# Kernel optimization log

Hardware: AMD Instinct MI355X
Metric: run time of the kernel (lower is better)

## Reference

```python
import jax, jax.numpy as jnp
import numpy as np

B, C, H, W = 4, 3, 512, 960
K2 = 16  # 4x4 adaptive filter, DAIN-style


def setup_inputs() -> dict:
    key = jax.random.key(0)
    k1, k2, k3 = jax.random.split(key, 3)
    teninput = jax.random.normal(k1, (B, C, H, W), dtype=jnp.float32)
    tenflow = jax.random.normal(k2, (B, 2, H, W), dtype=jnp.float32)
    tenfilter = jax.random.uniform(k3, (B, K2, H, W), dtype=jnp.float32)
    return {"teninput": teninput, "tenflow": tenflow, "tenfilter": tenfilter}


def reference(teninput, tenflow, tenfilter):
    # DAIN FilterInterpolation forward:
    # out[b,c,y,x] = valid * sum_{dj,di < K} filter[b, dj*K+di, y, x]
    #               * bilinear(input, y2_T + dj + beta, x2_L + di + alpha)
    # with per-corner clamped gathers; out-of-bounds flow targets give 0.
    b, c, h, w = teninput.shape
    k2 = tenfilter.shape[1]
    K = int(np.sqrt(k2))

    dt = teninput.dtype
    xs = jnp.arange(w, dtype=dt)[None, None, :]
    ys = jnp.arange(h, dtype=dt)[None, :, None]
    fx, fy = tenflow[:, 0], tenflow[:, 1]          # [B,H,W]
    x2 = xs + fx
    y2 = ys + fy
    valid = ((x2 >= 0) & (x2 <= w - 1) & (y2 >= 0) & (y2 <= h - 1)
             & (jnp.abs(fx) < w / 2) & (jnp.abs(fy) < h / 2))

    ix = jnp.floor(x2).astype(jnp.int32)
    iy = jnp.floor(y2).astype(jnp.int32)
    alpha = (x2 - ix)[:, None]                     # [B,1,H,W]
    beta = (y2 - iy)[:, None]
    ixL0 = ix + 1 - K // 2                         # window left edge
    iyT0 = iy + 1 - K // 2                         # window top edge

    inp_flat = teninput.reshape(b, c, h * w)

    def gather(yi, xi):  # yi, xi: [B,H,W] int -> [B,C,H,W]
        idx = (yi * w + xi).reshape(b, 1, h * w)
        return jnp.take_along_axis(inp_flat, idx, axis=2).reshape(b, c, h, w)

    wTL = (1 - alpha) * (1 - beta)
    wTR = alpha * (1 - beta)
    wBL = (1 - alpha) * beta
    wBR = alpha * beta

    out = jnp.zeros_like(teninput)
    for dj in range(K):
        yT = jnp.clip(iyT0 + dj, 0, h - 1)
        yB = jnp.clip(iyT0 + dj + 1, 0, h - 1)
        for di in range(K):
            xL = jnp.clip(ixL0 + di, 0, w - 1)
            xR = jnp.clip(ixL0 + di + 1, 0, w - 1)
            val = (wTL * gather(yT, xL) + wTR * gather(yT, xR)
                   + wBL * gather(yB, xL) + wBR * gather(yB, xR))
            out = out + val * tenfilter[:, dj * K + di][:, None]

    return out * valid[:, None].astype(dt)
```

## Files before the change

### kernel.cpp

```cpp
#include <hip/hip_runtime.h>

#define BB 4
#define CC 3
#define HH 512
#define WW 960
#define HW (HH * WW)
#define NPIX (BB * HW)

#define TW 64
#define TH 4
#define NTX (WW / TW)
#define NTY (HH / TH)
#define NBLK (BB * NTX * NTY)

#define ROWS 16
#define COLS 80
#define CPAD 84
#define LDS_FLOATS (ROWS * CC * CPAD)

__global__ __launch_bounds__(256)
void filter_interp_kernel(const float* __restrict__ inp,
                          const float* __restrict__ flow,
                          const float* __restrict__ filt,
                          float* __restrict__ out) {
    __shared__ float lds[LDS_FLOATS];

    const int bid = blockIdx.x;
    const int swz = (bid & 7) * (NBLK / 8) + (bid >> 3);
    const int b   = swz / (NTX * NTY);
    const int rr  = swz - b * (NTX * NTY);
    const int tx  = rr / NTY;
    const int ty  = rr - tx * NTY;
    const int x0  = tx * TW;
    const int y0  = ty * TH;

    const int tid = threadIdx.x;
    const float* ibase = inp + (size_t)b * CC * HW;

    if (tx > 0 && tx < NTX - 1) {
#pragma unroll
        for (int e = 0; e < 4; ++e) {
            const int idx = e * 256 + tid;
            if (idx < ROWS * CC * (COLS / 4)) {
                const int s  = idx / (CC * (COLS / 4));
                const int r2 = idx - s * (CC * (COLS / 4));
                const int ch = r2 / (COLS / 4);
                const int t4 = r2 - ch * (COLS / 4);
                const int grow = min(max(y0 - 5 + s, 0), HH - 1);
                const float4 v = *(const float4*)(ibase + (size_t)ch * HW +
                                                  (size_t)grow * WW +
                                                  (x0 - 8 + t4 * 4));
                *(float4*)&lds[(s * CC + ch) * CPAD + t4 * 4] = v;
            }
        }
    } else {
#pragma unroll
        for (int e = 0; e < 15; ++e) {
            const int idx = e * 256 + tid;
            const int s  = idx / (CC * COLS);
            const int r2 = idx - s * (CC * COLS);
            const int ch = r2 / COLS;
            const int t  = r2 - ch * COLS;
            const int grow = min(max(y0 - 5 + s, 0), HH - 1);
            const int gcol = min(max(x0 - 8 + t, 0), WW - 1);
            lds[(s * CC + ch) * CPAD + t] =
                ibase[(size_t)ch * HW + (size_t)grow * WW + gcol];
        }
    }

    const int lx = tid & (TW - 1);
    const int wy = tid >> 6;
    const int x  = x0 + lx;
    const int y  = y0 + wy;
    const int rem = y * WW + x;

    const float fx = flow[(size_t)(b * 2 + 0) * HW + rem];
    const float fy = flow[(size_t)(b * 2 + 1) * HW + rem];

    float f[16];
    {
        const float* fptr = filt + (size_t)b * 16 * HW + rem;
#pragma unroll
        for (int k = 0; k < 16; ++k) f[k] = fptr[(size_t)k * HW];
    }

    __syncthreads();

    const float x2 = (float)x + fx;
    const float y2 = (float)y + fy;

    const bool valid = (x2 >= 0.0f) && (x2 <= (float)(WW - 1)) &&
                       (y2 >= 0.0f) && (y2 <= (float)(HH - 1)) &&
                       (fabsf(fx) < (float)WW * 0.5f) &&
                       (fabsf(fy) < (float)HH * 0.5f);

    float acc0 = 0.0f, acc1 = 0.0f, acc2 = 0.0f;

    if (valid) {
        const int ix = (int)floorf(x2);
        const int iy = (int)floorf(y2);
        const float alpha = x2 - (float)ix;
        const float beta  = y2 - (float)iy;

        const float wTL = (1.0f - alpha) * (1.0f - beta);
        const float wTR = alpha * (1.0f - beta);
        const float wBL = (1.0f - alpha) * beta;
        const float wBR = alpha * beta;

        float Wm[5][5];
#pragma unroll
        for (int j = 0; j < 5; ++j)
#pragma unroll
            for (int i = 0; i < 5; ++i) Wm[j][i] = 0.0f;
#pragma unroll
        for (int dj = 0; dj < 4; ++dj) {
#pragma unroll
            for (int di = 0; di < 4; ++di) {
                const float fv = f[dj * 4 + di];
                Wm[dj][di]         += fv * wTL;
                Wm[dj][di + 1]     += fv * wTR;
                Wm[dj + 1][di]     += fv * wBL;
                Wm[dj + 1][di + 1] += fv * wBR;
            }
        }

        const int ixL0 = ix - 1;
        const int iyT0 = iy - 1;
        const int cs = ixL0 - (x0 - 8);
        const int rs = iyT0 - (y0 - 5);

        if ((unsigned)rs <= (unsigned)(ROWS - 5) &&
            (unsigned)cs <= (unsigned)(COLS - 5)) {
            const float* lbase = &lds[rs * (CC * CPAD) + cs];
#pragma unroll
            for (int j = 0; j < 5; ++j) {
                const float* lr = lbase + j * (CC * CPAD);
#pragma unroll
                for (int i = 0; i < 5; ++i) {
                    const float w = Wm[j][i];
                    acc0 += lr[i] * w;
                    acc1 += lr[CPAD + i] * w;
                    acc2 += lr[2 * CPAD + i] * w;
                }
            }
        } else {
            int R[5], S[5];
#pragma unroll
            for (int j = 0; j < 5; ++j) R[j] = min(max(iyT0 + j, 0), HH - 1);
#pragma unroll
            for (int i = 0; i < 5; ++i) S[i] = min(max(ixL0 + i, 0), WW - 1);
#pragma unroll
            for (int j = 0; j < 5; ++j) {
                const float* r0 = ibase + (size_t)R[j] * WW;
#pragma unroll
                for (int i = 0; i < 5; ++i) {
                    const float w = Wm[j][i];
                    const size_t o = (size_t)S[i];
                    acc0 += r0[o] * w;
                    acc1 += r0[HW + o] * w;
                    acc2 += r0[2 * (size_t)HW + o] * w;
                }
            }
        }
    }

    const int outbase = b * CC * HW + rem;
    out[outbase]          = acc0;
    out[outbase + HW]     = acc1;
    out[outbase + 2 * HW] = acc2;
}

extern "C" void kernel_launch(void* const* d_in, const int* in_sizes, int n_in,
                              void* d_out, int out_size, void* d_ws, size_t ws_size,
                              hipStream_t stream) {
    const float* teninput  = (const float*)d_in[0];
    const float* tenflow   = (const float*)d_in[1];
    const float* tenfilter = (const float*)d_in[2];
    float* out = (float*)d_out;

    filter_interp_kernel<<<NBLK, 256, 0, stream>>>(teninput, tenflow, tenfilter, out);
}
```

Baseline: 227.2 us.

## Stage input tile via global_load_lds and read LDS with aligned float2 taps

Interior tiles now copy the input halo straight from global memory into LDS with the gfx950 16-byte global_load_lds builtin, skipping the register round trip. To make that work, the LDS layout loses its row padding and becomes a dense row-by-channel-by-column array. The 5x5 gather from LDS is rewritten as three aligned float2 loads per row, covering 6 taps with the bilinear weights shifted by the column parity. This cuts LDS instruction count and staging overhead, but it adds one extra zero-weighted multiply per row and may bring more bank conflicts now that the padding is gone.

```diff
diff --git a/kernel.cpp b/kernel.cpp
--- a/kernel.cpp
+++ b/kernel.cpp
@@ -15,8 +15,11 @@
 
 #define ROWS 16
 #define COLS 80
-#define CPAD 84
-#define LDS_FLOATS (ROWS * CC * CPAD)
+#define RSTRIDE (CC * COLS)
+#define LDS_FLOATS (ROWS * RSTRIDE)
+
+typedef __attribute__((address_space(1))) const unsigned int gu32;
+typedef __attribute__((address_space(3))) unsigned int lu32;
 
 __global__ __launch_bounds__(256)
 void filter_interp_kernel(const float* __restrict__ inp,
@@ -34,7 +37,8 @@
     const int x0  = tx * TW;
     const int y0  = ty * TH;
 
-    const int tid = threadIdx.x;
+    const int tid  = threadIdx.x;
+    const int wave = tid >> 6;
     const float* ibase = inp + (size_t)b * CC * HW;
 
     if (tx > 0 && tx < NTX - 1) {
@@ -42,29 +46,29 @@
         for (int e = 0; e < 4; ++e) {
             const int idx = e * 256 + tid;
             if (idx < ROWS * CC * (COLS / 4)) {
-                const int s  = idx / (CC * (COLS / 4));
-                const int r2 = idx - s * (CC * (COLS / 4));
-                const int ch = r2 / (COLS / 4);
-                const int t4 = r2 - ch * (COLS / 4);
+                const int s  = idx / 60;
+                const int r2 = idx - s * 60;
+                const int ch = r2 / 20;
+                const int t4 = r2 - ch * 20;
                 const int grow = min(max(y0 - 5 + s, 0), HH - 1);
-                const float4 v = *(const float4*)(ibase + (size_t)ch * HW +
-                                                  (size_t)grow * WW +
-                                                  (x0 - 8 + t4 * 4));
-                *(float4*)&lds[(s * CC + ch) * CPAD + t4 * 4] = v;
+                const float* src = ibase + (size_t)ch * HW +
+                                   (size_t)grow * WW + (x0 - 8 + t4 * 4);
+                lu32* dst = (lu32*)(void*)&lds[(e * 256 + wave * 64) * 4];
+                __builtin_amdgcn_global_load_lds((gu32*)(const void*)src,
+                                                 dst, 16, 0, 0);
             }
         }
     } else {
 #pragma unroll
         for (int e = 0; e < 15; ++e) {
             const int idx = e * 256 + tid;
-            const int s  = idx / (CC * COLS);
-            const int r2 = idx - s * (CC * COLS);
+            const int s  = idx / RSTRIDE;
+            const int r2 = idx - s * RSTRIDE;
             const int ch = r2 / COLS;
             const int t  = r2 - ch * COLS;
             const int grow = min(max(y0 - 5 + s, 0), HH - 1);
             const int gcol = min(max(x0 - 8 + t, 0), WW - 1);
-            lds[(s * CC + ch) * CPAD + t] =
-                ibase[(size_t)ch * HW + (size_t)grow * WW + gcol];
+            lds[idx] = ibase[(size_t)ch * HW + (size_t)grow * WW + gcol];
         }
     }
 
@@ -131,34 +135,53 @@
 
         if ((unsigned)rs <= (unsigned)(ROWS - 5) &&
             (unsigned)cs <= (unsigned)(COLS - 5)) {
-            const float* lbase = &lds[rs * (CC * CPAD) + cs];
+            const int o  = cs & 1;
+            const int e0 = cs - o;
+            const float* lbase = &lds[rs * RSTRIDE + e0];
 #pragma unroll
             for (int j = 0; j < 5; ++j) {
-                const float* lr = lbase + j * (CC * CPAD);
+                const float* lr = lbase + j * RSTRIDE;
+                const float w0 = o ? 0.0f     : Wm[j][0];
+                const float w1 = o ? Wm[j][0] : Wm[j][1];
+                const float w2 = o ? Wm[j][1] : Wm[j][2];
+                const float w3 = o ? Wm[j][2] : Wm[j][3];
+                const float w4 = o ? Wm[j][3] : Wm[j][4];
+                const float w5 = o ? Wm[j][4] : 0.0f;
+
+                const float2 a0 = *(const float2*)(lr);
+                const float2 a1 = *(const float2*)(lr + 2);
+                const float2 a2 = *(const float2*)(lr + 4);
+                acc0 += a0.x * w0 + a0.y * w1 + a1.x * w2 +
+                        a1.y * w3 + a2.x * w4 + a2.y * w5;
+
+                const float2 b0 = *(const float2*)(lr + COLS);
+                const float2 b1 = *(const float2*)(lr + COLS + 2);
+                const float2 b2 = *(const float2*)(lr + COLS + 4);
+                acc1 += b0.x * w0 + b0.y * w1 + b1.x * w2 +
+                        b1.y * w3 + b2.x * w4 + b2.y * w5;
+
+                const float2 c0 = *(const float2*)(lr + 2 * COLS);
+                const float2 c1 = *(const float2*)(lr + 2 * COLS + 2);
+                const float2 c2 = *(const float2*)(lr + 2 * COLS + 4);
+                acc2 += c0.x * w0 + c0.y * w1 + c1.x * w2 +
+                        c1.y * w3 + c2.x * w4 + c2.y * w5;
+            }
+        } else {
+            int R[5], S[5];
+#pragma unroll
+            for (int j = 0; j < 5; ++j) R[j] = min(max(iyT0 + j, 0), HH - 1);
+#pragma unroll
+            for (int i = 0; i < 5; ++i) S[i] = min(max(ixL0 + i, 0), WW - 1);
+#pragma unroll
+            for (int j = 0; j < 5; ++j) {
+                const float* r0 = ibase + (size_t)R[j] * WW;
 #pragma unroll
                 for (int i = 0; i < 5; ++i) {
                     const float w = Wm[j][i];
-                    acc0 += lr[i] * w;
-                    acc1 += lr[CPAD + i] * w;
-                    acc2 += lr[2 * CPAD + i] * w;
-                }
-            }
-        } else {
-            int R[5], S[5];
-#pragma unroll
-            for (int j = 0; j < 5; ++j) R[j] = min(max(iyT0 + j, 0), HH - 1);
-#pragma unroll
-            for (int i = 0; i < 5; ++i) S[i] = min(max(ixL0 + i, 0), WW - 1);
-#pragma unroll
-            for (int j = 0; j < 5; ++j) {
-                const float* r0 = ibase + (size_t)R[j] * WW;
-#pragma unroll
-                for (int i = 0; i < 5; ++i) {
-                    const float w = Wm[j][i];
-                    const size_t o = (size_t)S[i];
-                    acc0 += r0[o] * w;
-                    acc1 += r0[HW + o] * w;
-                    acc2 += r0[2 * (size_t)HW + o] * w;
+                    const size_t oidx = (size_t)S[i];
+                    acc0 += r0[oidx] * w;
+                    acc1 += r0[HW + oidx] * w;
+                    acc2 += r0[2 * (size_t)HW + oidx] * w;
                 }
             }
         }
```

After: 220.4 us. 1.03x faster.
